# Performance work log

Hardware: AMD Instinct MI355X
Metric: run time of the kernel (lower is better)

The kernel has to match this reference:

```python
import jax, jax.numpy as jnp
import numpy as np
from jax import lax

B, S, L, E, H, V = 32, 64, 256, 64, 64, 6000


def setup_inputs() -> dict:
    key = jax.random.key(0)
    ks = jax.random.split(key, 8)
    inp = {
        "ids": jax.random.randint(ks[0], (B, S, L), 0, V, dtype=jnp.int32),
        "embed_table": jax.random.normal(ks[1], (V, E), jnp.float32) * 0.05,
        "Wk_f": jax.random.normal(ks[2], (E, 4 * H), jnp.float32) * 0.05,
        "Wr_f": jax.random.normal(ks[3], (H, 4 * H), jnp.float32) * 0.05,
        "b_f": jnp.zeros((4 * H,), jnp.float32),
        "Wk_b": jax.random.normal(ks[4], (E, 4 * H), jnp.float32) * 0.05,
        "Wr_b": jax.random.normal(ks[5], (H, 4 * H), jnp.float32) * 0.05,
        "b_b": jnp.zeros((4 * H,), jnp.float32),
    }
    return inp


def _lstm(xs, Wk, Wr, b):
    # xs: [L, N, E] -> hidden states [L, N, H]; Keras LSTM gate order i,f,c,o
    N = xs.shape[1]
    Hh = Wr.shape[0]
    pre = jnp.einsum('lne,eg->lng', xs, Wk) + b  # input projection once, outside scan

    def step(carry, zt):
        h, c = carry
        z = zt + h @ Wr
        i, f, g, o = jnp.split(z, 4, axis=-1)
        i = jax.nn.sigmoid(i)
        f = jax.nn.sigmoid(f)
        g = jnp.tanh(g)
        o = jax.nn.sigmoid(o)
        c = f * c + i * g
        h = o * jnp.tanh(c)
        return (h, c), h

    h0 = jnp.zeros((N, Hh), xs.dtype)
    _, hs = lax.scan(step, (h0, h0), pre)
    return hs


def reference(ids, embed_table, Wk_f, Wr_f, b_f, Wk_b, Wr_b, b_b):
    b, s, l = ids.shape
    e = embed_table.shape[1]
    h = Wr_f.shape[0]
    x = embed_table[ids]                      # [B,S,L,E]
    xs = x.reshape(b * s, l, e).transpose(1, 0, 2)  # [L, B*S, E]
    h_fwd = _lstm(xs, Wk_f, Wr_f, b_f)              # [L, N, H]
    h_bwd = _lstm(xs[::-1], Wk_b, Wr_b, b_b)[::-1]  # [L, N, H]
    out = jnp.concatenate([h_fwd, h_bwd], axis=-1)  # [L, N, 2H]
    return out.transpose(1, 0, 2).reshape(b, s, l, 2 * h)
```

## Files before the change

### kernel.cpp

```cpp
#include <hip/hip_runtime.h>

#define LL 256
#define EE 64
#define HH 64
#define GG 256
#define NSEQ 16
#define ROWP 72

typedef __bf16 bf16_t;
typedef bf16_t bf16x8 __attribute__((ext_vector_type(8)));
typedef float  f32x4  __attribute__((ext_vector_type(4)));

union BfPack {
    unsigned short u[8];
    bf16x8 v;
};

__device__ __forceinline__ unsigned short f2bf(float f) {
    unsigned u = __float_as_uint(f);
    u = (u + 0x7FFFu + ((u >> 16) & 1u)) >> 16;
    return (unsigned short)u;
}

#define LOG2E 1.44269504088896340736f

__device__ __forceinline__ float sigm(float x) {
    float e = __builtin_amdgcn_exp2f(-LOG2E * x);
    return __builtin_amdgcn_rcpf(1.0f + e);
}
__device__ __forceinline__ float tanh_fast(float x) {
    float t = fminf(fmaxf(x, -15.0f), 15.0f);
    float e = __builtin_amdgcn_exp2f((2.0f * LOG2E) * t);
    return 1.0f - 2.0f * __builtin_amdgcn_rcpf(e + 1.0f);
}

#define LGKM_BARRIER() asm volatile("s_waitcnt lgkmcnt(0)\n\ts_barrier" ::: "memory")

__global__ __launch_bounds__(256, 1)
void bilstm_mfma(const int* __restrict__ ids,
                 const float* __restrict__ embed,
                 const float* __restrict__ Wk_f, const float* __restrict__ Wr_f,
                 const float* __restrict__ b_f,
                 const float* __restrict__ Wk_b, const float* __restrict__ Wr_b,
                 const float* __restrict__ b_b,
                 float* __restrict__ out)
{
    const int dir = blockIdx.x >> 7;
    const int grp = blockIdx.x & 127;
    const int n0  = grp * NSEQ;
    const int tid  = threadIdx.x;
    const int w    = tid >> 6;
    const int lane = tid & 63;
    const int l15  = lane & 15;
    const int quad = lane >> 4;
    const int j    = w * 16 + l15;

    const float* Wk = dir ? Wk_b : Wk_f;
    const float* Wr = dir ? Wr_b : Wr_f;
    const float* bv = dir ? b_b  : b_f;

    __shared__ __align__(16) short s_x[2][NSEQ][ROWP];
    __shared__ __align__(16) short s_h[2][NSEQ][ROWP];
    __shared__ int s_ids[NSEQ][LL];

    for (int p = tid; p < NSEQ * LL; p += 256) {
        int m = p >> 8, t = p & 255;
        s_ids[m][t] = ids[(size_t)(n0 + m) * LL + t];
    }
    for (int p = tid; p < 2 * NSEQ * ROWP; p += 256)
        (&s_h[0][0][0])[p] = 0;

    __syncthreads();

    bf16x8 bfrag[4][4];
    f32x4  biasC[4];
    #pragma unroll
    for (int tt = 0; tt < 4; ++tt) {
        int g = tt * 64 + j;
        float bb = bv[g];
        biasC[tt] = (f32x4){bb, bb, bb, bb};
        #pragma unroll
        for (int kc = 0; kc < 4; ++kc) {
            BfPack pk;
            #pragma unroll
            for (int e = 0; e < 8; ++e) {
                int kg = kc * 32 + quad * 8 + e;
                float v = (kg < 64) ? Wk[(size_t)kg * GG + g]
                                    : Wr[(size_t)(kg - 64) * GG + g];
                pk.u[e] = f2bf(v);
            }
            bfrag[tt][kc] = pk.v;
        }
    }

    {
        int t0 = dir ? (LL - 1) : 0;
        #pragma unroll
        for (int u = 0; u < 2; ++u) {
            int pp = tid + u * 256;
            int m = pp >> 5, ep = pp & 31;
            int id = s_ids[m][t0];
            float2 xv = *(const float2*)&embed[(size_t)id * EE + 2 * ep];
            unsigned pk = (unsigned)f2bf(xv.x) | ((unsigned)f2bf(xv.y) << 16);
            *(unsigned*)&s_x[0][m][2 * ep] = pk;
        }
    }
    __syncthreads();

    float c[4] = {0.f, 0.f, 0.f, 0.f};
    const f32x4 zero4 = (f32x4){0.f, 0.f, 0.f, 0.f};

    for (int ts = 0; ts < LL; ++ts) {
        const int t  = dir ? (LL - 1 - ts) : ts;
        const int rb = ts & 1, wb = (ts + 1) & 1;

        float2 px0, px1;
        const int pm0 = tid >> 5, pe = tid & 31, pm1 = pm0 + 8;
        const bool pf = (ts + 1 < LL);
        if (pf) {
            int tn = dir ? (LL - 2 - ts) : (ts + 1);
            px0 = *(const float2*)&embed[(size_t)s_ids[pm0][tn] * EE + 2 * pe];
            px1 = *(const float2*)&embed[(size_t)s_ids[pm1][tn] * EE + 2 * pe];
        }

        bf16x8 ax0 = *(const bf16x8*)&s_x[rb][l15][quad * 8];
        bf16x8 ax1 = *(const bf16x8*)&s_x[rb][l15][32 + quad * 8];
        bf16x8 ah0 = *(const bf16x8*)&s_h[rb][l15][quad * 8];
        bf16x8 ah1 = *(const bf16x8*)&s_h[rb][l15][32 + quad * 8];

        f32x4 acc[4];
        #pragma unroll
        for (int tt = 0; tt < 4; ++tt) {
            f32x4 axc = __builtin_amdgcn_mfma_f32_16x16x32_bf16(ax0, bfrag[tt][0], biasC[tt], 0, 0, 0);
            axc = __builtin_amdgcn_mfma_f32_16x16x32_bf16(ax1, bfrag[tt][1], axc, 0, 0, 0);
            f32x4 ahc = __builtin_amdgcn_mfma_f32_16x16x32_bf16(ah0, bfrag[tt][2], zero4, 0, 0, 0);
            ahc = __builtin_amdgcn_mfma_f32_16x16x32_bf16(ah1, bfrag[tt][3], ahc, 0, 0, 0);
            acc[tt] = axc + ahc;
        }

        #pragma unroll
        for (int r = 0; r < 4; ++r) {
            float ig = sigm(acc[0][r]);
            float fg = sigm(acc[1][r]);
            float gg = tanh_fast(acc[2][r]);
            float og = sigm(acc[3][r]);
            c[r] = fg * c[r] + ig * gg;
            float hh = og * tanh_fast(c[r]);
            int m = quad * 4 + r;
            out[((size_t)(n0 + m) * LL + t) * (2 * HH) + dir * HH + j] = hh;
            s_h[wb][m][j] = (short)f2bf(hh);
        }

        if (pf) {
            unsigned pk0 = (unsigned)f2bf(px0.x) | ((unsigned)f2bf(px0.y) << 16);
            unsigned pk1 = (unsigned)f2bf(px1.x) | ((unsigned)f2bf(px1.y) << 16);
            *(unsigned*)&s_x[wb][pm0][2 * pe] = pk0;
            *(unsigned*)&s_x[wb][pm1][2 * pe] = pk1;
        }
        LGKM_BARRIER();
    }
}

extern "C" void kernel_launch(void* const* d_in, const int* in_sizes, int n_in,
                              void* d_out, int out_size, void* d_ws, size_t ws_size,
                              hipStream_t stream) {
    const int*   ids   = (const int*)d_in[0];
    const float* embed = (const float*)d_in[1];
    const float* Wk_f  = (const float*)d_in[2];
    const float* Wr_f  = (const float*)d_in[3];
    const float* b_f   = (const float*)d_in[4];
    const float* Wk_b  = (const float*)d_in[5];
    const float* Wr_b  = (const float*)d_in[6];
    const float* b_b   = (const float*)d_in[7];
    float* out = (float*)d_out;

    dim3 grid(256);
    dim3 block(256);
    bilstm_mfma<<<grid, block, 0, stream>>>(ids, embed,
                                            Wk_f, Wr_f, b_f,
                                            Wk_b, Wr_b, b_b,
                                            out);
}
```

Baseline: 415.2 us.

## Halve sequences per block to double grid and run two blocks per CU

Each block now handles 8 sequences instead of 16, padded to 16 MFMA rows, so the grid grows to 512 blocks and launch bounds allow two blocks per CU. The serial 256-step recurrence can then spread over more CUs or overlap across co-resident blocks, hiding barrier and latency stalls. Half of each MFMA's rows is now wasted on padding. The change also swaps manual bf16 rounding for the builtin conversion, drops the tanh input clamp, and replaces per-step output index math with incremented pointers.

```diff
diff --git a/kernel.cpp b/kernel.cpp
--- a/kernel.cpp
+++ b/kernel.cpp
@@ -4,7 +4,8 @@
 #define EE 64
 #define HH 64
 #define GG 256
-#define NSEQ 16
+#define NSEQ 8
+#define MROW 16
 #define ROWP 72
 
 typedef __bf16 bf16_t;
@@ -17,9 +18,7 @@
 };
 
 __device__ __forceinline__ unsigned short f2bf(float f) {
-    unsigned u = __float_as_uint(f);
-    u = (u + 0x7FFFu + ((u >> 16) & 1u)) >> 16;
-    return (unsigned short)u;
+    return __builtin_bit_cast(unsigned short, (__bf16)f);
 }
 
 #define LOG2E 1.44269504088896340736f
@@ -29,14 +28,13 @@
     return __builtin_amdgcn_rcpf(1.0f + e);
 }
 __device__ __forceinline__ float tanh_fast(float x) {
-    float t = fminf(fmaxf(x, -15.0f), 15.0f);
-    float e = __builtin_amdgcn_exp2f((2.0f * LOG2E) * t);
+    float e = __builtin_amdgcn_exp2f((2.0f * LOG2E) * x);
     return 1.0f - 2.0f * __builtin_amdgcn_rcpf(e + 1.0f);
 }
 
 #define LGKM_BARRIER() asm volatile("s_waitcnt lgkmcnt(0)\n\ts_barrier" ::: "memory")
 
-__global__ __launch_bounds__(256, 1)
+__global__ __launch_bounds__(256, 2)
 void bilstm_mfma(const int* __restrict__ ids,
                  const float* __restrict__ embed,
                  const float* __restrict__ Wk_f, const float* __restrict__ Wr_f,
@@ -45,8 +43,8 @@
                  const float* __restrict__ b_b,
                  float* __restrict__ out)
 {
-    const int dir = blockIdx.x >> 7;
-    const int grp = blockIdx.x & 127;
+    const int dir = blockIdx.x >> 8;
+    const int grp = blockIdx.x & 255;
     const int n0  = grp * NSEQ;
     const int tid  = threadIdx.x;
     const int w    = tid >> 6;
@@ -59,16 +57,18 @@
     const float* Wr = dir ? Wr_b : Wr_f;
     const float* bv = dir ? b_b  : b_f;
 
-    __shared__ __align__(16) short s_x[2][NSEQ][ROWP];
-    __shared__ __align__(16) short s_h[2][NSEQ][ROWP];
+    __shared__ __align__(16) short s_x[2][MROW][ROWP];
+    __shared__ __align__(16) short s_h[2][MROW][ROWP];
     __shared__ int s_ids[NSEQ][LL];
 
     for (int p = tid; p < NSEQ * LL; p += 256) {
         int m = p >> 8, t = p & 255;
         s_ids[m][t] = ids[(size_t)(n0 + m) * LL + t];
     }
-    for (int p = tid; p < 2 * NSEQ * ROWP; p += 256)
+    for (int p = tid; p < 2 * MROW * ROWP; p += 256) {
         (&s_h[0][0][0])[p] = 0;
+        (&s_x[0][0][0])[p] = 0;
+    }
 
     __syncthreads();
 
@@ -95,32 +95,38 @@
 
     {
         int t0 = dir ? (LL - 1) : 0;
-        #pragma unroll
-        for (int u = 0; u < 2; ++u) {
-            int pp = tid + u * 256;
-            int m = pp >> 5, ep = pp & 31;
-            int id = s_ids[m][t0];
-            float2 xv = *(const float2*)&embed[(size_t)id * EE + 2 * ep];
-            unsigned pk = (unsigned)f2bf(xv.x) | ((unsigned)f2bf(xv.y) << 16);
-            *(unsigned*)&s_x[0][m][2 * ep] = pk;
-        }
+        int m = tid >> 5, ep = tid & 31;
+        int id = s_ids[m][t0];
+        float2 xv = *(const float2*)&embed[(size_t)id * EE + 2 * ep];
+        unsigned pk = (unsigned)f2bf(xv.x) | ((unsigned)f2bf(xv.y) << 16);
+        *(unsigned*)&s_x[0][m][2 * ep] = pk;
     }
     __syncthreads();
 
     float c[4] = {0.f, 0.f, 0.f, 0.f};
     const f32x4 zero4 = (f32x4){0.f, 0.f, 0.f, 0.f};
 
+    const int tstep = dir ? -(2 * HH) : (2 * HH);
+    float* optr[4];
+    {
+        const int t0 = dir ? (LL - 1) : 0;
+        #pragma unroll
+        for (int r = 0; r < 4; ++r) {
+            int m = quad * 4 + r;
+            int mm = (m < NSEQ) ? m : 0;
+            optr[r] = out + ((size_t)(n0 + mm) * LL + t0) * (2 * HH) + dir * HH + j;
+        }
+    }
+
     for (int ts = 0; ts < LL; ++ts) {
-        const int t  = dir ? (LL - 1 - ts) : ts;
         const int rb = ts & 1, wb = (ts + 1) & 1;
 
-        float2 px0, px1;
-        const int pm0 = tid >> 5, pe = tid & 31, pm1 = pm0 + 8;
+        float2 px0;
+        const int pm0 = tid >> 5, pe = tid & 31;
         const bool pf = (ts + 1 < LL);
         if (pf) {
             int tn = dir ? (LL - 2 - ts) : (ts + 1);
             px0 = *(const float2*)&embed[(size_t)s_ids[pm0][tn] * EE + 2 * pe];
-            px1 = *(const float2*)&embed[(size_t)s_ids[pm1][tn] * EE + 2 * pe];
         }
 
         bf16x8 ax0 = *(const bf16x8*)&s_x[rb][l15][quad * 8];
@@ -146,16 +152,16 @@
             float og = sigm(acc[3][r]);
             c[r] = fg * c[r] + ig * gg;
             float hh = og * tanh_fast(c[r]);
-            int m = quad * 4 + r;
-            out[((size_t)(n0 + m) * LL + t) * (2 * HH) + dir * HH + j] = hh;
-            s_h[wb][m][j] = (short)f2bf(hh);
+            if (quad < 2) {
+                *optr[r] = hh;
+                s_h[wb][quad * 4 + r][j] = (short)f2bf(hh);
+            }
+            optr[r] += tstep;
         }
 
         if (pf) {
             unsigned pk0 = (unsigned)f2bf(px0.x) | ((unsigned)f2bf(px0.y) << 16);
-            unsigned pk1 = (unsigned)f2bf(px1.x) | ((unsigned)f2bf(px1.y) << 16);
             *(unsigned*)&s_x[wb][pm0][2 * pe] = pk0;
-            *(unsigned*)&s_x[wb][pm1][2 * pe] = pk1;
         }
         LGKM_BARRIER();
     }
@@ -174,7 +180,7 @@
     const float* b_b   = (const float*)d_in[7];
     float* out = (float*)d_out;
 
-    dim3 grid(256);
+    dim3 grid(512);
     dim3 block(256);
     bilstm_mfma<<<grid, block, 0, stream>>>(ids, embed,
                                             Wk_f, Wr_f, b_f,
```

After: 476.3 us. +14.7%, slower.
